# Optimization experiments

Measured on AMD Instinct MI355X. Metric: run time of the kernel, lower is better.

## Reference

```python
import jax, jax.numpy as jnp
import numpy as np

B, S, H, D = 2, 2048, 16, 128  # batch, seq, n_head, head_dim; n_embd = H*D
N_EMBD = H * D

def setup_inputs() -> dict:
    key = jax.random.key(0)
    kq, kk, kv = jax.random.split(key, 3)
    q = jax.random.normal(kq, (B, S, H, D), dtype=jnp.float32)
    k = jax.random.normal(kk, (B, S, H, D), dtype=jnp.float32)
    v = jax.random.normal(kv, (B, S, H, D), dtype=jnp.float32)
    return {"q": q, "k": k, "v": v}

def reference(q, k, v):
    # [B,S,H,D] -> [B,H,S,D]
    qh = jnp.transpose(q, (0, 2, 1, 3))
    kh = jnp.transpose(k, (0, 2, 1, 3))
    vh = jnp.transpose(v, (0, 2, 1, 3))
    # scores scaled by head_dim (NOT sqrt), matching the original module
    att = jnp.einsum('bhqd,bhkd->bhqk', qh, kh) / D
    att = jax.nn.softmax(att, axis=-1)
    y = jnp.einsum('bhqk,bhkd->bhqd', att, vh)
    # [B,H,S,D] -> [B,S,H,D] -> [B*S, n_embd]
    y = jnp.transpose(y, (0, 2, 1, 3)).reshape(B * S, N_EMBD)
    return y
```

## Files before the change

kernel.cpp:

```cpp
#include <hip/hip_runtime.h>


#define SEQ   2048
#define NHEAD 16
#define DH    128
#define NB    2
#define BQ    256
#define BK    64
#define NTHR  512
#define KSTR  136
#define VSTR  72
#define NKV   (SEQ / BK)
#define NELEM (NB * SEQ * NHEAD * DH)
#define KTILE (BK * KSTR)
#define VTILE (DH * VSTR)

typedef __attribute__((ext_vector_type(8)))  short bf16x8;
typedef __attribute__((ext_vector_type(16))) float f32x16;
typedef __attribute__((ext_vector_type(4)))  unsigned int u32x4;

__device__ __forceinline__ unsigned short f2bf(float x) {
    unsigned int u = __builtin_bit_cast(unsigned int, x);
    u += 0x7fffu + ((u >> 16) & 1u);
    return (unsigned short)(u >> 16);
}

__device__ __forceinline__ unsigned int bfr(float x) {
    unsigned int u = __builtin_bit_cast(unsigned int, x);
    return (u + 0x8000u) & 0xffff0000u;
}

__device__ __forceinline__ void pl32(unsigned int& a, unsigned int& b) {
    asm("v_permlane32_swap_b32 %0, %1" : "+v"(a), "+v"(b));
}

__global__ __launch_bounds__(256) void cvt_bf16(
    const float* __restrict__ q, const float* __restrict__ k,
    const float* __restrict__ v, unsigned short* __restrict__ dst)
{
    const int y = blockIdx.y;
    const float* s = (y == 0) ? q : (y == 1) ? k : v;
    unsigned short* d = dst + (size_t)y * NELEM;
    const int i = blockIdx.x * 256 + threadIdx.x;
    const float4 x = ((const float4*)s)[i];
    ushort4 o;
    o.x = f2bf(x.x); o.y = f2bf(x.y); o.z = f2bf(x.z); o.w = f2bf(x.w);
    ((ushort4*)d)[i] = o;
}

__global__ __launch_bounds__(NTHR, 2) void attn_fwd(
    const unsigned short* __restrict__ Qb,
    const unsigned short* __restrict__ Kb,
    const unsigned short* __restrict__ Vb,
    float* __restrict__ O)
{
    __shared__ unsigned short Kl[2][KTILE];
    __shared__ unsigned short Vl[2][VTILE];

    const int tid  = threadIdx.x;
    const int wave = tid >> 6;
    const int lane = tid & 63;
    const int hx   = lane >> 5;
    const int l32  = lane & 31;

    const int b  = blockIdx.y >> 4;
    const int h  = blockIdx.y & 15;
    const int q0 = blockIdx.x * BQ;

    const size_t rs = (size_t)NHEAD * DH;
    const unsigned short* qb = Qb + (size_t)b * SEQ * rs + (size_t)h * DH;
    const unsigned short* kb = Kb + (size_t)b * SEQ * rs + (size_t)h * DH;
    const unsigned short* vb = Vb + (size_t)b * SEQ * rs + (size_t)h * DH;

    bf16x8 qf[8];
    {
        const unsigned short* qp = qb + (size_t)(q0 + wave * 32 + l32) * rs + hx * 8;
        #pragma unroll
        for (int c = 0; c < 8; ++c)
            qf[c] = *(const bf16x8*)(qp + c * 16);
    }

    int kgo[2], kls[2];
    #pragma unroll
    for (int p = 0; p < 2; ++p) {
        const int cidx = p * NTHR + tid;
        const int key  = cidx >> 4;
        const int cc   = cidx & 15;
        kgo[p] = key * (int)rs + cc * 8;
        kls[p] = key * KSTR + cc * 8;
    }
    const int kp  = tid & 31;
    const int dcv = tid >> 5;

    f32x16 o4[4];
    #pragma unroll
    for (int t = 0; t < 4; ++t)
        #pragma unroll
        for (int r = 0; r < 16; ++r) o4[t][r] = 0.f;
    float lsum = 0.f;
    const float c1 = 1.44269504088896340736f / 128.0f;

    bf16x8 kr[2], vr[2];

    {
        #pragma unroll
        for (int p = 0; p < 2; ++p) kr[p] = *(const bf16x8*)(kb + kgo[p]);
        {
            const unsigned short* src = vb + (size_t)(2 * kp) * rs + dcv * 8;
            vr[0] = *(const bf16x8*)src;
            vr[1] = *(const bf16x8*)(src + rs);
        }
        #pragma unroll
        for (int p = 0; p < 2; ++p) *(bf16x8*)&Kl[0][kls[p]] = kr[p];
        unsigned int* vw = (unsigned int*)&Vl[0][0];
        #pragma unroll
        for (int j = 0; j < 8; ++j) {
            const unsigned int pr = ((unsigned int)(unsigned short)vr[0][j])
                                  | (((unsigned int)(unsigned short)vr[1][j]) << 16);
            vw[(dcv * 8 + j) * (VSTR / 2) + kp] = pr;
        }
    }
    __syncthreads();

    for (int kv = 0; kv < NKV; ++kv) {
        const int cur = kv & 1;
        const int k0n = ((kv + 1) & (NKV - 1)) * BK;

        #pragma unroll
        for (int p = 0; p < 2; ++p) kr[p] = *(const bf16x8*)(kb + (size_t)k0n * rs + kgo[p]);
        {
            const unsigned short* src = vb + (size_t)(k0n + 2 * kp) * rs + dcv * 8;
            vr[0] = *(const bf16x8*)src;
            vr[1] = *(const bf16x8*)(src + rs);
        }

        const unsigned short* Kc = &Kl[cur][0];
        const unsigned short* Vc = &Vl[cur][0];

        #pragma unroll
        for (int kt = 0; kt < 2; ++kt) {
            f32x16 s;
            #pragma unroll
            for (int r = 0; r < 16; ++r) s[r] = 0.f;
            #pragma unroll
            for (int c = 0; c < 8; ++c) {
                bf16x8 kf = *(const bf16x8*)&Kc[(kt * 32 + l32) * KSTR + c * 16 + hx * 8];
                s = __builtin_amdgcn_mfma_f32_32x32x16_bf16(kf, qf[c], s, 0, 0, 0);
            }

            unsigned int w[4][2];
            #pragma unroll
            for (int g = 0; g < 4; ++g) {
                const unsigned int u0 = bfr(__builtin_amdgcn_exp2f(s[g * 4 + 0] * c1));
                const unsigned int u1 = bfr(__builtin_amdgcn_exp2f(s[g * 4 + 1] * c1));
                const unsigned int u2 = bfr(__builtin_amdgcn_exp2f(s[g * 4 + 2] * c1));
                const unsigned int u3 = bfr(__builtin_amdgcn_exp2f(s[g * 4 + 3] * c1));
                lsum += (__builtin_bit_cast(float, u0) + __builtin_bit_cast(float, u1))
                      + (__builtin_bit_cast(float, u2) + __builtin_bit_cast(float, u3));
                w[g][0] = u1 | (u0 >> 16);
                w[g][1] = u3 | (u2 >> 16);
            }

            #pragma unroll
            for (int ks = 0; ks < 2; ++ks) {
                pl32(w[2 * ks][0], w[2 * ks + 1][0]);
                pl32(w[2 * ks][1], w[2 * ks + 1][1]);
            }
            bf16x8 pf[2];
            #pragma unroll
            for (int ks = 0; ks < 2; ++ks) {
                u32x4 t;
                t.x = w[2 * ks][0];
                t.y = w[2 * ks][1];
                t.z = w[2 * ks + 1][0];
                t.w = w[2 * ks + 1][1];
                pf[ks] = __builtin_bit_cast(bf16x8, t);
            }

            #pragma unroll
            for (int ks = 0; ks < 2; ++ks)
                #pragma unroll
                for (int dt = 0; dt < 4; ++dt) {
                    bf16x8 vf = *(const bf16x8*)&Vc[(dt * 32 + l32) * VSTR
                                                    + kt * 32 + ks * 16 + hx * 8];
                    o4[dt] = __builtin_amdgcn_mfma_f32_32x32x16_bf16(pf[ks], vf, o4[dt], 0, 0, 0);
                }
        }

        const int nxt = cur ^ 1;
        #pragma unroll
        for (int p = 0; p < 2; ++p) *(bf16x8*)&Kl[nxt][kls[p]] = kr[p];
        {
            unsigned int* vw = (unsigned int*)&Vl[nxt][0];
            #pragma unroll
            for (int j = 0; j < 8; ++j) {
                const unsigned int pr = ((unsigned int)(unsigned short)vr[0][j])
                                      | (((unsigned int)(unsigned short)vr[1][j]) << 16);
                vw[(dcv * 8 + j) * (VSTR / 2) + kp] = pr;
            }
        }
        __syncthreads();
    }

    lsum += __shfl_xor(lsum, 32, 64);
    const float inv = 1.0f / lsum;
    float iv[16];
    #pragma unroll
    for (int r = 0; r < 16; ++r)
        iv[r] = __shfl(inv, (r & 3) + 8 * (r >> 2) + 4 * hx, 64);

    #pragma unroll
    for (int dt = 0; dt < 4; ++dt) {
        #pragma unroll
        for (int r = 0; r < 16; ++r) {
            const int ql = (r & 3) + 8 * (r >> 2) + 4 * hx;
            const int qg = q0 + wave * 32 + ql;
            O[(size_t)(b * SEQ + qg) * rs + (size_t)h * DH + dt * 32 + l32] = o4[dt][r] * iv[r];
        }
    }
}

extern "C" void kernel_launch(void* const* d_in, const int* in_sizes, int n_in,
                              void* d_out, int out_size, void* d_ws, size_t ws_size,
                              hipStream_t stream) {
    const float* q = (const float*)d_in[0];
    const float* k = (const float*)d_in[1];
    const float* v = (const float*)d_in[2];
    float* o = (float*)d_out;
    unsigned short* wsb = (unsigned short*)d_ws;

    cvt_bf16<<<dim3(NELEM / 1024, 3), 256, 0, stream>>>(q, k, v, wsb);
    attn_fwd<<<dim3(SEQ / BQ, NB * NHEAD), dim3(NTHR), 0, stream>>>(
        wsb, wsb + NELEM, wsb + 2 * (size_t)NELEM, o);
}
```

Measured before the change: 208.9 us.

## Fuse fp32-to-bf16 conversion into attention kernel loads, drop separate cast pass

Removes the standalone cvt_bf16 kernel and has the attention kernel read fp32 Q/K/V directly from global memory. It converts them to bf16 in registers with v_cvt_pk_bf16_f32 before writing the K/V tiles to LDS. This saves one kernel launch and a full read-write pass over all three tensors. In exchange, each attention block now reads twice as many bytes per K/V tile, and K/V are re-read by the 8 query blocks per head, which adds global traffic and register pressure inside the main loop.

New measurement: 231.1 us. +10.6%, slower.

```diff
diff --git a/kernel.cpp b/kernel.cpp
--- a/kernel.cpp
+++ b/kernel.cpp
@@ -11,7 +11,6 @@
 #define KSTR  136
 #define VSTR  72
 #define NKV   (SEQ / BK)
-#define NELEM (NB * SEQ * NHEAD * DH)
 #define KTILE (BK * KSTR)
 #define VTILE (DH * VSTR)
 
@@ -19,39 +18,25 @@
 typedef __attribute__((ext_vector_type(16))) float f32x16;
 typedef __attribute__((ext_vector_type(4)))  unsigned int u32x4;
 
-__device__ __forceinline__ unsigned short f2bf(float x) {
-    unsigned int u = __builtin_bit_cast(unsigned int, x);
-    u += 0x7fffu + ((u >> 16) & 1u);
-    return (unsigned short)(u >> 16);
-}
-
 __device__ __forceinline__ unsigned int bfr(float x) {
     unsigned int u = __builtin_bit_cast(unsigned int, x);
     return (u + 0x8000u) & 0xffff0000u;
 }
 
+__device__ __forceinline__ unsigned int cpk(float lo, float hi) {
+    unsigned int d;
+    asm("v_cvt_pk_bf16_f32 %0, %1, %2" : "=v"(d) : "v"(lo), "v"(hi));
+    return d;
+}
+
 __device__ __forceinline__ void pl32(unsigned int& a, unsigned int& b) {
     asm("v_permlane32_swap_b32 %0, %1" : "+v"(a), "+v"(b));
 }
 
-__global__ __launch_bounds__(256) void cvt_bf16(
-    const float* __restrict__ q, const float* __restrict__ k,
-    const float* __restrict__ v, unsigned short* __restrict__ dst)
-{
-    const int y = blockIdx.y;
-    const float* s = (y == 0) ? q : (y == 1) ? k : v;
-    unsigned short* d = dst + (size_t)y * NELEM;
-    const int i = blockIdx.x * 256 + threadIdx.x;
-    const float4 x = ((const float4*)s)[i];
-    ushort4 o;
-    o.x = f2bf(x.x); o.y = f2bf(x.y); o.z = f2bf(x.z); o.w = f2bf(x.w);
-    ((ushort4*)d)[i] = o;
-}
-
 __global__ __launch_bounds__(NTHR, 2) void attn_fwd(
-    const unsigned short* __restrict__ Qb,
-    const unsigned short* __restrict__ Kb,
-    const unsigned short* __restrict__ Vb,
+    const float* __restrict__ Qb,
+    const float* __restrict__ Kb,
+    const float* __restrict__ Vb,
     float* __restrict__ O)
 {
     __shared__ unsigned short Kl[2][KTILE];
@@ -68,16 +53,22 @@
     const int q0 = blockIdx.x * BQ;
 
     const size_t rs = (size_t)NHEAD * DH;
-    const unsigned short* qb = Qb + (size_t)b * SEQ * rs + (size_t)h * DH;
-    const unsigned short* kb = Kb + (size_t)b * SEQ * rs + (size_t)h * DH;
-    const unsigned short* vb = Vb + (size_t)b * SEQ * rs + (size_t)h * DH;
+    const float* qb = Qb + (size_t)b * SEQ * rs + (size_t)h * DH;
+    const float* kb = Kb + (size_t)b * SEQ * rs + (size_t)h * DH;
+    const float* vb = Vb + (size_t)b * SEQ * rs + (size_t)h * DH;
 
     bf16x8 qf[8];
     {
-        const unsigned short* qp = qb + (size_t)(q0 + wave * 32 + l32) * rs + hx * 8;
-        #pragma unroll
-        for (int c = 0; c < 8; ++c)
-            qf[c] = *(const bf16x8*)(qp + c * 16);
+        const float* qp = qb + (size_t)(q0 + wave * 32 + l32) * rs + hx * 8;
+        #pragma unroll
+        for (int c = 0; c < 8; ++c) {
+            const float4 a  = *(const float4*)(qp + c * 16);
+            const float4 b2 = *(const float4*)(qp + c * 16 + 4);
+            u32x4 t;
+            t.x = cpk(a.x,  a.y);  t.y = cpk(a.z,  a.w);
+            t.z = cpk(b2.x, b2.y); t.w = cpk(b2.z, b2.w);
+            qf[c] = __builtin_bit_cast(bf16x8, t);
+        }
     }
 
     int kgo[2], kls[2];
@@ -100,25 +91,36 @@
     float lsum = 0.f;
     const float c1 = 1.44269504088896340736f / 128.0f;
 
-    bf16x8 kr[2], vr[2];
+    float4 krA[2], krB[2];
+    float4 vr0a, vr0b, vr1a, vr1b;
 
     {
         #pragma unroll
-        for (int p = 0; p < 2; ++p) kr[p] = *(const bf16x8*)(kb + kgo[p]);
+        for (int p = 0; p < 2; ++p) {
+            krA[p] = *(const float4*)(kb + kgo[p]);
+            krB[p] = *(const float4*)(kb + kgo[p] + 4);
+        }
         {
-            const unsigned short* src = vb + (size_t)(2 * kp) * rs + dcv * 8;
-            vr[0] = *(const bf16x8*)src;
-            vr[1] = *(const bf16x8*)(src + rs);
-        }
-        #pragma unroll
-        for (int p = 0; p < 2; ++p) *(bf16x8*)&Kl[0][kls[p]] = kr[p];
+            const float* src = vb + (size_t)(2 * kp) * rs + dcv * 8;
+            vr0a = *(const float4*)src;        vr0b = *(const float4*)(src + 4);
+            vr1a = *(const float4*)(src + rs); vr1b = *(const float4*)(src + rs + 4);
+        }
+        #pragma unroll
+        for (int p = 0; p < 2; ++p) {
+            u32x4 t;
+            t.x = cpk(krA[p].x, krA[p].y); t.y = cpk(krA[p].z, krA[p].w);
+            t.z = cpk(krB[p].x, krB[p].y); t.w = cpk(krB[p].z, krB[p].w);
+            *(u32x4*)&Kl[0][kls[p]] = t;
+        }
         unsigned int* vw = (unsigned int*)&Vl[0][0];
-        #pragma unroll
-        for (int j = 0; j < 8; ++j) {
-            const unsigned int pr = ((unsigned int)(unsigned short)vr[0][j])
-                                  | (((unsigned int)(unsigned short)vr[1][j]) << 16);
-            vw[(dcv * 8 + j) * (VSTR / 2) + kp] = pr;
-        }
+        vw[(dcv * 8 + 0) * (VSTR / 2) + kp] = cpk(vr0a.x, vr1a.x);
+        vw[(dcv * 8 + 1) * (VSTR / 2) + kp] = cpk(vr0a.y, vr1a.y);
+        vw[(dcv * 8 + 2) * (VSTR / 2) + kp] = cpk(vr0a.z, vr1a.z);
+        vw[(dcv * 8 + 3) * (VSTR / 2) + kp] = cpk(vr0a.w, vr1a.w);
+        vw[(dcv * 8 + 4) * (VSTR / 2) + kp] = cpk(vr0b.x, vr1b.x);
+        vw[(dcv * 8 + 5) * (VSTR / 2) + kp] = cpk(vr0b.y, vr1b.y);
+        vw[(dcv * 8 + 6) * (VSTR / 2) + kp] = cpk(vr0b.z, vr1b.z);
+        vw[(dcv * 8 + 7) * (VSTR / 2) + kp] = cpk(vr0b.w, vr1b.w);
     }
     __syncthreads();
 
@@ -127,11 +129,14 @@
         const int k0n = ((kv + 1) & (NKV - 1)) * BK;
 
         #pragma unroll
-        for (int p = 0; p < 2; ++p) kr[p] = *(const bf16x8*)(kb + (size_t)k0n * rs + kgo[p]);
+        for (int p = 0; p < 2; ++p) {
+            krA[p] = *(const float4*)(kb + (size_t)k0n * rs + kgo[p]);
+            krB[p] = *(const float4*)(kb + (size_t)k0n * rs + kgo[p] + 4);
+        }
         {
-            const unsigned short* src = vb + (size_t)(k0n + 2 * kp) * rs + dcv * 8;
-            vr[0] = *(const bf16x8*)src;
-            vr[1] = *(const bf16x8*)(src + rs);
+            const float* src = vb + (size_t)(k0n + 2 * kp) * rs + dcv * 8;
+            vr0a = *(const float4*)src;        vr0b = *(const float4*)(src + 4);
+            vr1a = *(const float4*)(src + rs); vr1b = *(const float4*)(src + rs + 4);
         }
 
         const unsigned short* Kc = &Kl[cur][0];
@@ -189,15 +194,22 @@
 
         const int nxt = cur ^ 1;
         #pragma unroll
-        for (int p = 0; p < 2; ++p) *(bf16x8*)&Kl[nxt][kls[p]] = kr[p];
+        for (int p = 0; p < 2; ++p) {
+            u32x4 t;
+            t.x = cpk(krA[p].x, krA[p].y); t.y = cpk(krA[p].z, krA[p].w);
+            t.z = cpk(krB[p].x, krB[p].y); t.w = cpk(krB[p].z, krB[p].w);
+            *(u32x4*)&Kl[nxt][kls[p]] = t;
+        }
         {
             unsigned int* vw = (unsigned int*)&Vl[nxt][0];
-            #pragma unroll
-            for (int j = 0; j < 8; ++j) {
-                const unsigned int pr = ((unsigned int)(unsigned short)vr[0][j])
-                                      | (((unsigned int)(unsigned short)vr[1][j]) << 16);
-                vw[(dcv * 8 + j) * (VSTR / 2) + kp] = pr;
-            }
+            vw[(dcv * 8 + 0) * (VSTR / 2) + kp] = cpk(vr0a.x, vr1a.x);
+            vw[(dcv * 8 + 1) * (VSTR / 2) + kp] = cpk(vr0a.y, vr1a.y);
+            vw[(dcv * 8 + 2) * (VSTR / 2) + kp] = cpk(vr0a.z, vr1a.z);
+            vw[(dcv * 8 + 3) * (VSTR / 2) + kp] = cpk(vr0a.w, vr1a.w);
+            vw[(dcv * 8 + 4) * (VSTR / 2) + kp] = cpk(vr0b.x, vr1b.x);
+            vw[(dcv * 8 + 5) * (VSTR / 2) + kp] = cpk(vr0b.y, vr1b.y);
+            vw[(dcv * 8 + 6) * (VSTR / 2) + kp] = cpk(vr0b.z, vr1b.z);
+            vw[(dcv * 8 + 7) * (VSTR / 2) + kp] = cpk(vr0b.w, vr1b.w);
         }
         __syncthreads();
     }
@@ -227,9 +239,7 @@
     const float* k = (const float*)d_in[1];
     const float* v = (const float*)d_in[2];
     float* o = (float*)d_out;
-    unsigned short* wsb = (unsigned short*)d_ws;
-
-    cvt_bf16<<<dim3(NELEM / 1024, 3), 256, 0, stream>>>(q, k, v, wsb);
-    attn_fwd<<<dim3(SEQ / BQ, NB * NHEAD), dim3(NTHR), 0, stream>>>(
-        wsb, wsb + NELEM, wsb + 2 * (size_t)NELEM, o);
-}
+    (void)d_ws; (void)ws_size;
+
+    attn_fwd<<<dim3(SEQ / BQ, NB * NHEAD), dim3(NTHR), 0, stream>>>(q, k, v, o);
+}
```

## Convert Q to bf16 inside attention kernel and remap block-to-head assignment

Applied to the files above, without the earlier changes.

Drops the Q tensor from the separate fp32-to-bf16 conversion pass, so the attention kernel now loads fp32 Q directly and packs it with v_cvt_pk_bf16_f32. This removes one third of the conversion kernel's global reads and writes. Block indices are also remapped so that consecutive blocks are spread across different heads, which is likely meant to balance L2 and XCD locality for the K/V reads. The trade-off is that each attention block reads twice as many bytes for Q, and the conversion uses round-to-nearest-even via hardware.

Result: faster. 199.8 us (-4.4%).

```diff
diff --git a/kernel.cpp b/kernel.cpp
--- a/kernel.cpp
+++ b/kernel.cpp
@@ -30,16 +30,22 @@
     return (u + 0x8000u) & 0xffff0000u;
 }
 
+__device__ __forceinline__ unsigned int cpk(float lo, float hi) {
+    unsigned int d;
+    asm("v_cvt_pk_bf16_f32 %0, %1, %2" : "=v"(d) : "v"(lo), "v"(hi));
+    return d;
+}
+
 __device__ __forceinline__ void pl32(unsigned int& a, unsigned int& b) {
     asm("v_permlane32_swap_b32 %0, %1" : "+v"(a), "+v"(b));
 }
 
 __global__ __launch_bounds__(256) void cvt_bf16(
-    const float* __restrict__ q, const float* __restrict__ k,
-    const float* __restrict__ v, unsigned short* __restrict__ dst)
+    const float* __restrict__ k, const float* __restrict__ v,
+    unsigned short* __restrict__ dst)
 {
     const int y = blockIdx.y;
-    const float* s = (y == 0) ? q : (y == 1) ? k : v;
+    const float* s = (y == 0) ? k : v;
     unsigned short* d = dst + (size_t)y * NELEM;
     const int i = blockIdx.x * 256 + threadIdx.x;
     const float4 x = ((const float4*)s)[i];
@@ -49,7 +55,7 @@
 }
 
 __global__ __launch_bounds__(NTHR, 2) void attn_fwd(
-    const unsigned short* __restrict__ Qb,
+    const float* __restrict__ Qb,
     const unsigned short* __restrict__ Kb,
     const unsigned short* __restrict__ Vb,
     float* __restrict__ O)
@@ -63,21 +69,31 @@
     const int hx   = lane >> 5;
     const int l32  = lane & 31;
 
-    const int b  = blockIdx.y >> 4;
-    const int h  = blockIdx.y & 15;
-    const int q0 = blockIdx.x * BQ;
+    const int bid = blockIdx.x + (int)(blockIdx.y << 3);
+    const int xk  = bid & 7;
+    const int j   = bid >> 3;
+    const int hc  = (xk << 2) + (j >> 3);
+    const int b   = hc >> 4;
+    const int h   = hc & 15;
+    const int q0  = (j & 7) * BQ;
 
     const size_t rs = (size_t)NHEAD * DH;
-    const unsigned short* qb = Qb + (size_t)b * SEQ * rs + (size_t)h * DH;
+    const float*          qb = Qb + (size_t)b * SEQ * rs + (size_t)h * DH;
     const unsigned short* kb = Kb + (size_t)b * SEQ * rs + (size_t)h * DH;
     const unsigned short* vb = Vb + (size_t)b * SEQ * rs + (size_t)h * DH;
 
     bf16x8 qf[8];
     {
-        const unsigned short* qp = qb + (size_t)(q0 + wave * 32 + l32) * rs + hx * 8;
-        #pragma unroll
-        for (int c = 0; c < 8; ++c)
-            qf[c] = *(const bf16x8*)(qp + c * 16);
+        const float* qp = qb + (size_t)(q0 + wave * 32 + l32) * rs + hx * 8;
+        #pragma unroll
+        for (int c = 0; c < 8; ++c) {
+            const float4 a  = *(const float4*)(qp + c * 16);
+            const float4 b2 = *(const float4*)(qp + c * 16 + 4);
+            u32x4 t;
+            t.x = cpk(a.x,  a.y);  t.y = cpk(a.z,  a.w);
+            t.z = cpk(b2.x, b2.y); t.w = cpk(b2.z, b2.w);
+            qf[c] = __builtin_bit_cast(bf16x8, t);
+        }
     }
 
     int kgo[2], kls[2];
@@ -114,10 +130,10 @@
         for (int p = 0; p < 2; ++p) *(bf16x8*)&Kl[0][kls[p]] = kr[p];
         unsigned int* vw = (unsigned int*)&Vl[0][0];
         #pragma unroll
-        for (int j = 0; j < 8; ++j) {
-            const unsigned int pr = ((unsigned int)(unsigned short)vr[0][j])
-                                  | (((unsigned int)(unsigned short)vr[1][j]) << 16);
-            vw[(dcv * 8 + j) * (VSTR / 2) + kp] = pr;
+        for (int j2 = 0; j2 < 8; ++j2) {
+            const unsigned int pr = ((unsigned int)(unsigned short)vr[0][j2])
+                                  | (((unsigned int)(unsigned short)vr[1][j2]) << 16);
+            vw[(dcv * 8 + j2) * (VSTR / 2) + kp] = pr;
         }
     }
     __syncthreads();
@@ -193,10 +209,10 @@
         {
             unsigned int* vw = (unsigned int*)&Vl[nxt][0];
             #pragma unroll
-            for (int j = 0; j < 8; ++j) {
-                const unsigned int pr = ((unsigned int)(unsigned short)vr[0][j])
-                                      | (((unsigned int)(unsigned short)vr[1][j]) << 16);
-                vw[(dcv * 8 + j) * (VSTR / 2) + kp] = pr;
+            for (int j2 = 0; j2 < 8; ++j2) {
+                const unsigned int pr = ((unsigned int)(unsigned short)vr[0][j2])
+                                      | (((unsigned int)(unsigned short)vr[1][j2]) << 16);
+                vw[(dcv * 8 + j2) * (VSTR / 2) + kp] = pr;
             }
         }
         __syncthreads();
@@ -229,7 +245,7 @@
     float* o = (float*)d_out;
     unsigned short* wsb = (unsigned short*)d_ws;
 
-    cvt_bf16<<<dim3(NELEM / 1024, 3), 256, 0, stream>>>(q, k, v, wsb);
+    cvt_bf16<<<dim3(NELEM / 1024, 2), 256, 0, stream>>>(k, v, wsb);
     attn_fwd<<<dim3(SEQ / BQ, NB * NHEAD), dim3(NTHR), 0, stream>>>(
-        wsb, wsb + NELEM, wsb + 2 * (size_t)NELEM, o);
-}
+        q, wsb, wsb + NELEM, o);
+}
```
